# Performance work log

Measured on AMD Instinct MI355X. Metric: run time of the kernel, lower is better.

The kernel has to match this reference:

```python
import jax, jax.numpy as jnp
import numpy as np

N_NODES = 100000
N_EDGES = 3200000


def gcn_conv(x, src, dst, W, b, num_nodes):
    """PyG-style GCNConv: symmetric-normalized aggregation with self-loops."""
    h = x @ W  # [N, out]
    # add self loops
    loop = jnp.arange(num_nodes, dtype=src.dtype)
    s = jnp.concatenate([src, loop])
    d = jnp.concatenate([dst, loop])
    deg = jax.ops.segment_sum(jnp.ones_like(d, dtype=h.dtype), d, num_segments=num_nodes)
    dinv = jnp.where(deg > 0, jax.lax.rsqrt(deg), 0.0)
    norm = dinv[s] * dinv[d]  # [E+N]
    msg = h[s] * norm[:, None]  # gather + scale
    out = jax.ops.segment_sum(msg, d, num_segments=num_nodes)  # scatter-add
    return out + b


def setup_inputs() -> dict:
    key = jax.random.key(0)
    ks = jax.random.split(key, 8)
    x = jax.random.normal(ks[0], (N_NODES, 8), dtype=jnp.float32)
    edge_index = jax.random.randint(ks[1], (2, N_EDGES), 0, N_NODES, dtype=jnp.int64)
    W1 = jax.random.normal(ks[2], (8, 64), dtype=jnp.float32) * 0.3
    b1 = jnp.zeros((64,), dtype=jnp.float32)
    W2 = jax.random.normal(ks[3], (64, 32), dtype=jnp.float32) * 0.12
    b2 = jnp.zeros((32,), dtype=jnp.float32)
    conv_w = jax.random.normal(ks[4], (16, 32, 3), dtype=jnp.float32) * 0.1
    conv_b = jnp.zeros((16,), dtype=jnp.float32)
    fc_w = jax.random.normal(ks[5], (16, 22), dtype=jnp.float32) * 0.25
    fc_b = jnp.zeros((22,), dtype=jnp.float32)
    return {"x": x, "edge_index": edge_index, "W1": W1, "b1": b1, "W2": W2,
            "b2": b2, "conv_w": conv_w, "conv_b": conv_b, "fc_w": fc_w, "fc_b": fc_b}


def reference(x, edge_index, W1, b1, W2, b2, conv_w, conv_b, fc_w, fc_b):
    src, dst = edge_index[0], edge_index[1]
    h = jax.nn.elu(gcn_conv(x, src, dst, W1, b1, N_NODES))   # [N, 64]
    h = jax.nn.elu(gcn_conv(h, src, dst, W2, b2, N_NODES))   # [N, 32]
    # Conv1d(32,16,3) over the node axis: [1, C=32, L=N]
    hc = h.T[None]  # [1, 32, N]
    y = jax.lax.conv_general_dilated(hc, conv_w, window_strides=(1,),
                                     padding='VALID',
                                     dimension_numbers=('NCH', 'OIH', 'NCH'))
    y = jax.nn.relu(y + conv_b[None, :, None])  # [1, 16, N-2]
    y = y[0].T  # [N-2, 16]
    return y @ fc_w + fc_b  # [N-2, 22]
```

## Files before the change

kernel.cpp:

```cpp
#include <hip/hip_runtime.h>
#include <hip/hip_fp16.h>
#include <math.h>

#define BKT_SHIFT 8
#define BKT_NODES 256
#define HROWS 64

__global__ __launch_bounds__(256) void k_hist(const int* __restrict__ dst,
                                              int* __restrict__ bcnt, int E, int NB) {
    __shared__ int lh[512];
    for (int i = threadIdx.x; i < NB; i += 256) lh[i] = 0;
    __syncthreads();
    int base = blockIdx.x * 4096;
    if (base + 4096 <= E) {
        const int4* d4 = (const int4*)(dst + base);
#pragma unroll
        for (int k = 0; k < 4; ++k) {
            int4 v = d4[k * 256 + threadIdx.x];
            atomicAdd(&lh[v.x >> BKT_SHIFT], 1);
            atomicAdd(&lh[v.y >> BKT_SHIFT], 1);
            atomicAdd(&lh[v.z >> BKT_SHIFT], 1);
            atomicAdd(&lh[v.w >> BKT_SHIFT], 1);
        }
    } else {
        for (int k = 0; k < 16; ++k) {
            int i = base + k * 256 + threadIdx.x;
            if (i < E) atomicAdd(&lh[dst[i] >> BKT_SHIFT], 1);
        }
    }
    __syncthreads();
    for (int i = threadIdx.x; i < NB; i += 256)
        if (lh[i]) atomicAdd(&bcnt[i], lh[i]);
}

__global__ __launch_bounds__(512) void k_bscan(const int* __restrict__ bc,
                                               int* __restrict__ boff,
                                               int* __restrict__ bcur, int NB, int E) {
    __shared__ int s[512];
    __shared__ int carry;
    if (threadIdx.x == 0) carry = 0;
    __syncthreads();
    for (int base = 0; base < NB; base += 512) {
        int i = base + threadIdx.x;
        int v = (i < NB) ? bc[i] : 0;
        s[threadIdx.x] = v;
        __syncthreads();
        for (int off = 1; off < 512; off <<= 1) {
            int t = (threadIdx.x >= off) ? s[threadIdx.x - off] : 0;
            __syncthreads();
            s[threadIdx.x] += t;
            __syncthreads();
        }
        if (i < NB) {
            int ex = carry + s[threadIdx.x] - v;
            boff[i] = ex;
            bcur[i] = ex;
        }
        __syncthreads();
        if (threadIdx.x == 0) carry += s[511];
        __syncthreads();
    }
    if (threadIdx.x == 0) boff[NB] = E;
}

__global__ __launch_bounds__(1024) void k_part(const int* __restrict__ src,
                                               const int* __restrict__ dst,
                                               int* __restrict__ bcur,
                                               int* __restrict__ ebuf, int E, int NB) {
    __shared__ int lh[512];
    for (int i = threadIdx.x; i < NB; i += 1024) lh[i] = 0;
    __syncthreads();
    int base = blockIdx.x * 8192;
    if (base + 8192 <= E) {
        const int4* d4 = (const int4*)(dst + base);
#pragma unroll
        for (int k = 0; k < 2; ++k) {
            int4 v = d4[k * 1024 + threadIdx.x];
            atomicAdd(&lh[v.x >> BKT_SHIFT], 1);
            atomicAdd(&lh[v.y >> BKT_SHIFT], 1);
            atomicAdd(&lh[v.z >> BKT_SHIFT], 1);
            atomicAdd(&lh[v.w >> BKT_SHIFT], 1);
        }
    } else {
        for (int k = 0; k < 8; ++k) {
            int i = base + k * 1024 + threadIdx.x;
            if (i < E) atomicAdd(&lh[dst[i] >> BKT_SHIFT], 1);
        }
    }
    __syncthreads();
    for (int t = threadIdx.x; t < NB; t += 1024) {
        int c = lh[t];
        lh[t] = c ? atomicAdd(&bcur[t], c) : 0;
    }
    __syncthreads();
    if (base + 8192 <= E) {
        const int4* d4 = (const int4*)(dst + base);
        const int4* s4 = (const int4*)(src + base);
#pragma unroll
        for (int k = 0; k < 2; ++k) {
            int4 dv = d4[k * 1024 + threadIdx.x];
            int4 sv = s4[k * 1024 + threadIdx.x];
            int p;
            p = atomicAdd(&lh[dv.x >> BKT_SHIFT], 1); ebuf[p] = ((dv.x & 255) << 24) | sv.x;
            p = atomicAdd(&lh[dv.y >> BKT_SHIFT], 1); ebuf[p] = ((dv.y & 255) << 24) | sv.y;
            p = atomicAdd(&lh[dv.z >> BKT_SHIFT], 1); ebuf[p] = ((dv.z & 255) << 24) | sv.z;
            p = atomicAdd(&lh[dv.w >> BKT_SHIFT], 1); ebuf[p] = ((dv.w & 255) << 24) | sv.w;
        }
    } else {
        for (int k = 0; k < 8; ++k) {
            int i = base + k * 1024 + threadIdx.x;
            if (i < E) {
                int d = dst[i];
                int p = atomicAdd(&lh[d >> BKT_SHIFT], 1);
                ebuf[p] = ((d & 255) << 24) | src[i];
            }
        }
    }
}

__global__ __launch_bounds__(256) void k_lsort(const int* __restrict__ boff,
                                               const int* __restrict__ ebuf,
                                               const float* __restrict__ x,
                                               int* __restrict__ rowstart,
                                               float* __restrict__ dinv,
                                               __half2* __restrict__ hx,
                                               int* __restrict__ csr, int n, int NB) {
    __shared__ int off[256];
    __shared__ int cnt[256];
    int b = blockIdx.x;
    int start = boff[b], end = boff[b + 1];
    cnt[threadIdx.x] = 0;
    __syncthreads();
    for (int i = start + threadIdx.x; i < end; i += 256)
        atomicAdd(&cnt[((unsigned)ebuf[i]) >> 24], 1);
    __syncthreads();
    int v = cnt[threadIdx.x];
    off[threadIdx.x] = v;
    __syncthreads();
    for (int o = 1; o < 256; o <<= 1) {
        int t = (threadIdx.x >= o) ? off[threadIdx.x - o] : 0;
        __syncthreads();
        off[threadIdx.x] += t;
        __syncthreads();
    }
    int excl = off[threadIdx.x] - v;
    int node = (b << BKT_SHIFT) + threadIdx.x;
    if (node < n) {
        rowstart[node] = start + excl;
        float dv = rsqrtf((float)v + 1.0f);
        dinv[node] = dv;
        const float4* xp = (const float4*)(x + (size_t)node * 8);
        float4 a = xp[0], c = xp[1];
        __half2* hp = hx + (size_t)node * 4;
        hp[0] = __floats2half2_rn(a.x * dv, a.y * dv);
        hp[1] = __floats2half2_rn(a.z * dv, a.w * dv);
        hp[2] = __floats2half2_rn(c.x * dv, c.y * dv);
        hp[3] = __floats2half2_rn(c.z * dv, c.w * dv);
    }
    __syncthreads();
    off[threadIdx.x] = excl;
    __syncthreads();
    for (int i = start + threadIdx.x; i < end; i += 256) {
        int rec = ebuf[i];
        int d = ((unsigned)rec) >> 24;
        int pos = atomicAdd(&off[d], 1);
        csr[start + pos] = rec & 0xFFFFFF;
    }
    if (b == NB - 1 && threadIdx.x == 0) rowstart[n] = end;
}

__global__ __launch_bounds__(256) void k_agg1g(const int* __restrict__ rs, const int* __restrict__ csr,
                                               const float* __restrict__ dinv, const __half2* __restrict__ hx,
                                               const float* __restrict__ W1, const float* __restrict__ bias,
                                               const float* __restrict__ W2, __half* __restrict__ hw2, int n) {
    __shared__ float w[512];
    __shared__ float sb[64];
    __shared__ float w2s[64 * 36];
    for (int i = threadIdx.x; i < 512; i += 256) w[i] = W1[i];
    if (threadIdx.x < 64) sb[threadIdx.x] = bias[threadIdx.x];
    for (int i = threadIdx.x; i < 2048; i += 256) {
        int r = i >> 5, c = i & 31;
        w2s[r * 36 + c] = W2[i];
    }
    __syncthreads();
    int wid = (blockIdx.x * 256 + threadIdx.x) >> 2;
    if (wid >= n) return;
    int jp = threadIdx.x & 3;
    int start = rs[wid], end = rs[wid + 1];
    float ax = 0.f, ay = 0.f;
    for (int i = start; i < end; i += 16) {
        int idx[16];
        float msk[16];
#pragma unroll
        for (int k = 0; k < 16; ++k) {
            int ii = i + k;
            bool ok = ii < end;
            idx[k] = ok ? csr[ii] : wid;
            msk[k] = ok ? 1.f : 0.f;
        }
        float2 f[16];
#pragma unroll
        for (int k = 0; k < 16; ++k)
            f[k] = __half22float2(hx[((size_t)idx[k] << 2) + jp]);
#pragma unroll
        for (int k = 0; k < 16; ++k) {
            ax = fmaf(msk[k], f[k].x, ax);
            ay = fmaf(msk[k], f[k].y, ay);
        }
    }
    {
        float2 f = __half22float2(hx[((size_t)wid << 2) + jp]);
        ax += f.x; ay += f.y;
    }
    float bx = __shfl_xor(ax, 1), by = __shfl_xor(ay, 1);
    float cx = __shfl_xor(ax, 2), cy = __shfl_xor(ay, 2);
    float dx = __shfl_xor(bx, 2), dy = __shfl_xor(by, 2);
    float dv = dinv[wid];
    int fb = jp * 16;
    const float* r0 = &w[(2 * jp) * 64 + fb];          const float* r1 = r0 + 64;
    const float* r2 = &w[(2 * (jp ^ 1)) * 64 + fb];    const float* r3 = r2 + 64;
    const float* r4 = &w[(2 * (jp ^ 2)) * 64 + fb];    const float* r5 = r4 + 64;
    const float* r6 = &w[(2 * (jp ^ 3)) * 64 + fb];    const float* r7 = r6 + 64;
    const float* sbp = &sb[fb];
    float4 o4[4];
#pragma unroll
    for (int m4 = 0; m4 < 4; ++m4) {
        float4 wa = *(const float4*)&r0[m4 * 4];
        float4 wb = *(const float4*)&r1[m4 * 4];
        float4 wc = *(const float4*)&r2[m4 * 4];
        float4 wd = *(const float4*)&r3[m4 * 4];
        float4 we = *(const float4*)&r4[m4 * 4];
        float4 wf = *(const float4*)&r5[m4 * 4];
        float4 wg = *(const float4*)&r6[m4 * 4];
        float4 wh = *(const float4*)&r7[m4 * 4];
        float4 o;
        o.x = dv * (ax * wa.x + ay * wb.x + bx * wc.x + by * wd.x + cx * we.x + cy * wf.x + dx * wg.x + dy * wh.x) + sbp[m4 * 4 + 0];
        o.y = dv * (ax * wa.y + ay * wb.y + bx * wc.y + by * wd.y + cx * we.y + cy * wf.y + dx * wg.y + dy * wh.y) + sbp[m4 * 4 + 1];
        o.z = dv * (ax * wa.z + ay * wb.z + bx * wc.z + by * wd.z + cx * we.z + cy * wf.z + dx * wg.z + dy * wh.z) + sbp[m4 * 4 + 2];
        o.w = dv * (ax * wa.w + ay * wb.w + bx * wc.w + by * wd.w + cx * we.w + cy * wf.w + dx * wg.w + dy * wh.w) + sbp[m4 * 4 + 3];
        o.x = o.x > 0.f ? o.x : expm1f(o.x);
        o.y = o.y > 0.f ? o.y : expm1f(o.y);
        o.z = o.z > 0.f ? o.z : expm1f(o.z);
        o.w = o.w > 0.f ? o.w : expm1f(o.w);
        o4[m4] = o;
    }
    float4 acc[8];
#pragma unroll
    for (int j4 = 0; j4 < 8; ++j4) acc[j4] = make_float4(0.f, 0.f, 0.f, 0.f);
#pragma unroll
    for (int m4 = 0; m4 < 4; ++m4) {
        int mm = (m4 + jp) & 3;
        float4 ov;
        {
            float4 t0 = (mm & 2) ? o4[2] : o4[0];
            float4 t1 = (mm & 2) ? o4[3] : o4[1];
            ov = (mm & 1) ? t1 : t0;
        }
#pragma unroll
        for (int q = 0; q < 4; ++q) {
            float om = q == 0 ? ov.x : q == 1 ? ov.y : q == 2 ? ov.z : ov.w;
            const float4* wr = (const float4*)&w2s[(fb + mm * 4 + q) * 36];
#pragma unroll
            for (int j4 = 0; j4 < 8; ++j4) {
                float4 wv = wr[j4];
                acc[j4].x = fmaf(om, wv.x, acc[j4].x);
                acc[j4].y = fmaf(om, wv.y, acc[j4].y);
                acc[j4].z = fmaf(om, wv.z, acc[j4].z);
                acc[j4].w = fmaf(om, wv.w, acc[j4].w);
            }
        }
    }
    bool hi1 = (jp & 1) != 0;
    float4 keep1[4];
#pragma unroll
    for (int i = 0; i < 4; ++i) {
        float4 lo = acc[i], hi = acc[i + 4];
        float4 mine, send;
        mine.x = hi1 ? hi.x : lo.x;  send.x = hi1 ? lo.x : hi.x;
        mine.y = hi1 ? hi.y : lo.y;  send.y = hi1 ? lo.y : hi.y;
        mine.z = hi1 ? hi.z : lo.z;  send.z = hi1 ? lo.z : hi.z;
        mine.w = hi1 ? hi.w : lo.w;  send.w = hi1 ? lo.w : hi.w;
        mine.x += __shfl_xor(send.x, 1);
        mine.y += __shfl_xor(send.y, 1);
        mine.z += __shfl_xor(send.z, 1);
        mine.w += __shfl_xor(send.w, 1);
        keep1[i] = mine;
    }
    bool hi2 = (jp & 2) != 0;
    float4 fin[2];
#pragma unroll
    for (int i = 0; i < 2; ++i) {
        float4 lo = keep1[i], hi = keep1[i + 2];
        float4 mine, send;
        mine.x = hi2 ? hi.x : lo.x;  send.x = hi2 ? lo.x : hi.x;
        mine.y = hi2 ? hi.y : lo.y;  send.y = hi2 ? lo.y : hi.y;
        mine.z = hi2 ? hi.z : lo.z;  send.z = hi2 ? lo.z : hi.z;
        mine.w = hi2 ? hi.w : lo.w;  send.w = hi2 ? lo.w : hi.w;
        mine.x += __shfl_xor(send.x, 2);
        mine.y += __shfl_xor(send.y, 2);
        mine.z += __shfl_xor(send.z, 2);
        mine.w += __shfl_xor(send.w, 2);
        fin[i] = mine;
    }
    int jb = (jp & 1) * 16 + (jp & 2) * 4;
    __half2 h01 = __floats2half2_rn(fin[0].x * dv, fin[0].y * dv);
    __half2 h23 = __floats2half2_rn(fin[0].z * dv, fin[0].w * dv);
    __half2 h45 = __floats2half2_rn(fin[1].x * dv, fin[1].y * dv);
    __half2 h67 = __floats2half2_rn(fin[1].z * dv, fin[1].w * dv);
    uint4 u;
    u.x = *(unsigned*)&h01; u.y = *(unsigned*)&h23;
    u.z = *(unsigned*)&h45; u.w = *(unsigned*)&h67;
    *(uint4*)((char*)hw2 + (size_t)wid * 64 + jb * 2) = u;
}

__global__ __launch_bounds__(256) void k_aggr32p(const int* __restrict__ rs, const int* __restrict__ csr,
                                                 const float* __restrict__ dinv, const __half* __restrict__ hw,
                                                 const float* __restrict__ bias, float* __restrict__ g, int n) {
    int wid = (blockIdx.x * 256 + threadIdx.x) >> 4;
    if (wid >= n) return;
    int j = threadIdx.x & 15;
    int start = rs[wid], end = rs[wid + 1];
    const __half2* hp = (const __half2*)hw;
    float ax = 0.f, ay = 0.f;
    for (int i = start; i < end; i += 16) {
        int idx[16];
        float msk[16];
#pragma unroll
        for (int k = 0; k < 16; ++k) {
            int ii = i + k;
            bool ok = ii < end;
            idx[k] = ok ? csr[ii] : wid;
            msk[k] = ok ? 1.f : 0.f;
        }
        float2 f[16];
#pragma unroll
        for (int k = 0; k < 16; ++k)
            f[k] = __half22float2(hp[((size_t)idx[k] << 4) + j]);
#pragma unroll
        for (int k = 0; k < 16; ++k) {
            ax = fmaf(msk[k], f[k].x, ax);
            ay = fmaf(msk[k], f[k].y, ay);
        }
    }
    float dv = dinv[wid];
    float2 fs = __half22float2(hp[((size_t)wid << 4) + j]);
    float2 bb = ((const float2*)bias)[j];
    float vx = dv * (ax + fs.x) + bb.x;
    float vy = dv * (ay + fs.y) + bb.y;
    float2 r;
    r.x = vx > 0.f ? vx : expm1f(vx);
    r.y = vy > 0.f ? vy : expm1f(vy);
    ((float2*)(g + ((size_t)wid << 5)))[j] = r;
}

__global__ __launch_bounds__(256) void k_head(const float* __restrict__ g2, const float* __restrict__ cw,
                                              const float* __restrict__ cb, const float* __restrict__ fw,
                                              const float* __restrict__ fb, float* __restrict__ out,
                                              int nrows) {
    __shared__ float tile[(HROWS + 2) * 36];
    __shared__ float scwT[96 * 16];
    __shared__ float ytile[HROWS * 20];
    __shared__ float sfwT[22 * 16];
    __shared__ float scb[16], sfb[22];
    int base = blockIdx.x * HROWS;
    int rcnt = nrows - base; if (rcnt > HROWS) rcnt = HROWS;
    for (int i = threadIdx.x; i < 1536; i += 256) {
        int co = i / 96, rem = i - co * 96;
        scwT[rem * 16 + co] = cw[i];
    }
    for (int i = threadIdx.x; i < 352; i += 256) {
        int co = i / 22, col = i - co * 22;
        sfwT[col * 16 + co] = fw[i];
    }
    if (threadIdx.x < 16) scb[threadIdx.x] = cb[threadIdx.x];
    if (threadIdx.x < 22) sfb[threadIdx.x] = fb[threadIdx.x];
    int nload4 = (rcnt + 2) * 8;
    for (int i = threadIdx.x; i < nload4; i += 256) {
        int r = i >> 3, c4 = i & 7;
        float4 v = *(const float4*)(g2 + (size_t)(base + r) * 32 + c4 * 4);
        *(float4*)&tile[r * 36 + c4 * 4] = v;
    }
    __syncthreads();
    int r = threadIdx.x >> 2;
    int c0 = threadIdx.x & 3;
    if (r < rcnt) {
        float4 acc = { scb[c0 * 4], scb[c0 * 4 + 1], scb[c0 * 4 + 2], scb[c0 * 4 + 3] };
#pragma unroll
        for (int k = 0; k < 3; ++k) {
            const float* tr = &tile[(r + k) * 36];
#pragma unroll
            for (int ci4 = 0; ci4 < 8; ++ci4) {
                float4 xv = *(const float4*)&tr[ci4 * 4];
#pragma unroll
                for (int q = 0; q < 4; ++q) {
                    int ci = ci4 * 4 + q;
                    float4 wv = *(const float4*)&scwT[(ci * 3 + k) * 16 + c0 * 4];
                    float xq = q == 0 ? xv.x : q == 1 ? xv.y : q == 2 ? xv.z : xv.w;
                    acc.x += xq * wv.x;
                    acc.y += xq * wv.y;
                    acc.z += xq * wv.z;
                    acc.w += xq * wv.w;
                }
            }
        }
        float4 yv;
        yv.x = acc.x > 0.f ? acc.x : 0.f;
        yv.y = acc.y > 0.f ? acc.y : 0.f;
        yv.z = acc.z > 0.f ? acc.z : 0.f;
        yv.w = acc.w > 0.f ? acc.w : 0.f;
        *(float4*)&ytile[r * 20 + c0 * 4] = yv;
    }
    __syncthreads();
    int items = rcnt * 22;
    for (int it = threadIdx.x; it < items; it += 256) {
        int row = it / 22, col = it - row * 22;
        const float* yr = &ytile[row * 20];
        const float* wc = &sfwT[col * 16];
        float s = sfb[col];
#pragma unroll
        for (int co4 = 0; co4 < 4; ++co4) {
            float4 yv = *(const float4*)&yr[co4 * 4];
            float4 wv = *(const float4*)&wc[co4 * 4];
            s += yv.x * wv.x + yv.y * wv.y + yv.z * wv.z + yv.w * wv.w;
        }
        out[(size_t)base * 22 + it] = s;
    }
}

extern "C" void kernel_launch(void* const* d_in, const int* in_sizes, int n_in,
                              void* d_out, int out_size, void* d_ws, size_t ws_size,
                              hipStream_t stream) {
    const float* x  = (const float*)d_in[0];
    const int*   ei = (const int*)d_in[1];
    const float* W1 = (const float*)d_in[2];
    const float* b1 = (const float*)d_in[3];
    const float* W2 = (const float*)d_in[4];
    const float* b2 = (const float*)d_in[5];
    const float* cw = (const float*)d_in[6];
    const float* cb = (const float*)d_in[7];
    const float* fw = (const float*)d_in[8];
    const float* fb = (const float*)d_in[9];
    float* out = (float*)d_out;

    int N = in_sizes[0] / 8;
    int E = in_sizes[1] / 2;
    const int* src = ei;
    const int* dst = ei + E;
    int NB = (N + BKT_NODES - 1) >> BKT_SHIFT;

    auto alignB = [](size_t v) { return (v + 1023) & ~(size_t)1023; };
    char* wsb = (char*)d_ws;
    size_t o = 0;
    int* bcnt = (int*)(wsb + o);      o += 2048;
    int* boff = (int*)(wsb + o);      o += 2048;
    int* bcur = (int*)(wsb + o);      o += 2048;
    int* rowstart = (int*)(wsb + o);  o += alignB((size_t)(N + 1) * 4);
    float* dinv = (float*)(wsb + o);  o += alignB((size_t)N * 4);
    int* csr = (int*)(wsb + o);       o += alignB((size_t)E * 4 + 256);
    __half2* hx = (__half2*)(wsb + o);  o += alignB((size_t)N * 8 * 2);
    __half* hw2 = (__half*)(wsb + o);   o += alignB((size_t)N * 32 * 2);
    float* B = (float*)(wsb + o);     o += (size_t)N * 64 * 4;
    int* ebuf = (int*)B;

    hipMemsetAsync(bcnt, 0, (size_t)NB * sizeof(int), stream);
    k_hist<<<(E + 4095) / 4096, 256, 0, stream>>>(dst, bcnt, E, NB);
    k_bscan<<<1, 512, 0, stream>>>(bcnt, boff, bcur, NB, E);
    k_part<<<(E + 8191) / 8192, 1024, 0, stream>>>(src, dst, bcur, ebuf, E, NB);
    k_lsort<<<NB, 256, 0, stream>>>(boff, ebuf, x, rowstart, dinv, hx, csr, N, NB);

    k_agg1g<<<(int)(((size_t)N * 4 + 255) / 256), 256, 0, stream>>>(rowstart, csr, dinv, hx, W1, b1, W2, hw2, N);

    k_aggr32p<<<(int)(((size_t)N * 16 + 255) / 256), 256, 0, stream>>>(rowstart, csr, dinv, hw2, b2, B, N);

    k_head<<<(N - 2 + HROWS - 1) / HROWS, 256, 0, stream>>>(B, cw, cb, fw, fb, out, N - 2);
}
```

Baseline: 172.1 us.

## Fuse second GCN aggregation with conv1d and FC head kernel

```diff
diff --git a/kernel.cpp b/kernel.cpp
--- a/kernel.cpp
+++ b/kernel.cpp
@@ -4,7 +4,7 @@
 
 #define BKT_SHIFT 8
 #define BKT_NODES 256
-#define HROWS 64
+#define HB 16
 
 __global__ __launch_bounds__(256) void k_hist(const int* __restrict__ dst,
                                               int* __restrict__ bcnt, int E, int NB) {
@@ -313,106 +313,85 @@
     *(uint4*)((char*)hw2 + (size_t)wid * 64 + jb * 2) = u;
 }
 
-__global__ __launch_bounds__(256) void k_aggr32p(const int* __restrict__ rs, const int* __restrict__ csr,
-                                                 const float* __restrict__ dinv, const __half* __restrict__ hw,
-                                                 const float* __restrict__ bias, float* __restrict__ g, int n) {
-    int wid = (blockIdx.x * 256 + threadIdx.x) >> 4;
-    if (wid >= n) return;
-    int j = threadIdx.x & 15;
-    int start = rs[wid], end = rs[wid + 1];
-    const __half2* hp = (const __half2*)hw;
-    float ax = 0.f, ay = 0.f;
-    for (int i = start; i < end; i += 16) {
-        int idx[16];
-        float msk[16];
-#pragma unroll
-        for (int k = 0; k < 16; ++k) {
-            int ii = i + k;
-            bool ok = ii < end;
-            idx[k] = ok ? csr[ii] : wid;
-            msk[k] = ok ? 1.f : 0.f;
-        }
-        float2 f[16];
-#pragma unroll
-        for (int k = 0; k < 16; ++k)
-            f[k] = __half22float2(hp[((size_t)idx[k] << 4) + j]);
-#pragma unroll
-        for (int k = 0; k < 16; ++k) {
-            ax = fmaf(msk[k], f[k].x, ax);
-            ay = fmaf(msk[k], f[k].y, ay);
-        }
-    }
-    float dv = dinv[wid];
-    float2 fs = __half22float2(hp[((size_t)wid << 4) + j]);
-    float2 bb = ((const float2*)bias)[j];
-    float vx = dv * (ax + fs.x) + bb.x;
-    float vy = dv * (ay + fs.y) + bb.y;
-    float2 r;
-    r.x = vx > 0.f ? vx : expm1f(vx);
-    r.y = vy > 0.f ? vy : expm1f(vy);
-    ((float2*)(g + ((size_t)wid << 5)))[j] = r;
-}
-
-__global__ __launch_bounds__(256) void k_head(const float* __restrict__ g2, const float* __restrict__ cw,
-                                              const float* __restrict__ cb, const float* __restrict__ fw,
-                                              const float* __restrict__ fb, float* __restrict__ out,
-                                              int nrows) {
-    __shared__ float tile[(HROWS + 2) * 36];
+__global__ __launch_bounds__(320) void k_agg2h(const int* __restrict__ rs, const int* __restrict__ csr,
+                                               const float* __restrict__ dinv, const __half* __restrict__ hw,
+                                               const float* __restrict__ bias,
+                                               const float* __restrict__ cw, const float* __restrict__ cb,
+                                               const float* __restrict__ fw, const float* __restrict__ fb,
+                                               float* __restrict__ out, int n, int nrows) {
+    __shared__ float tile[18 * 36];
     __shared__ float scwT[96 * 16];
-    __shared__ float ytile[HROWS * 20];
+    __shared__ float ytile[16 * 20];
     __shared__ float sfwT[22 * 16];
-    __shared__ float scb[16], sfb[22];
-    int base = blockIdx.x * HROWS;
-    int rcnt = nrows - base; if (rcnt > HROWS) rcnt = HROWS;
-    for (int i = threadIdx.x; i < 1536; i += 256) {
+    __shared__ float scb[16], sfb[22], sbb[32];
+    for (int i = threadIdx.x; i < 1536; i += 320) {
         int co = i / 96, rem = i - co * 96;
         scwT[rem * 16 + co] = cw[i];
     }
-    for (int i = threadIdx.x; i < 352; i += 256) {
+    for (int i = threadIdx.x; i < 352; i += 320) {
         int co = i / 22, col = i - co * 22;
         sfwT[col * 16 + co] = fw[i];
     }
     if (threadIdx.x < 16) scb[threadIdx.x] = cb[threadIdx.x];
     if (threadIdx.x < 22) sfb[threadIdx.x] = fb[threadIdx.x];
-    int nload4 = (rcnt + 2) * 8;
-    for (int i = threadIdx.x; i < nload4; i += 256) {
-        int r = i >> 3, c4 = i & 7;
-        float4 v = *(const float4*)(g2 + (size_t)(base + r) * 32 + c4 * 4);
-        *(float4*)&tile[r * 36 + c4 * 4] = v;
-    }
-    __syncthreads();
-    int r = threadIdx.x >> 2;
-    int c0 = threadIdx.x & 3;
-    if (r < rcnt) {
-        float4 acc = { scb[c0 * 4], scb[c0 * 4 + 1], scb[c0 * 4 + 2], scb[c0 * 4 + 3] };
-#pragma unroll
-        for (int k = 0; k < 3; ++k) {
-            const float* tr = &tile[(r + k) * 36];
-#pragma unroll
-            for (int ci4 = 0; ci4 < 8; ++ci4) {
-                float4 xv = *(const float4*)&tr[ci4 * 4];
-#pragma unroll
-                for (int q = 0; q < 4; ++q) {
-                    int ci = ci4 * 4 + q;
-                    float4 wv = *(const float4*)&scwT[(ci * 3 + k) * 16 + c0 * 4];
-                    float xq = q == 0 ? xv.x : q == 1 ? xv.y : q == 2 ? xv.z : xv.w;
-                    acc.x += xq * wv.x;
-                    acc.y += xq * wv.y;
-                    acc.z += xq * wv.z;
-                    acc.w += xq * wv.w;
-                }
+    if (threadIdx.x < 32) sbb[threadIdx.x] = bias[threadIdx.x];
+    __syncthreads();
+    int base = blockIdx.x * HB;
+    int slot = threadIdx.x >> 4;
+    int j = threadIdx.x & 15;
+    int wid = base + slot;
+    if (slot < 18 && wid < n) {
+        int start = rs[wid], end = rs[wid + 1];
+        const __half2* hp = (const __half2*)hw;
+        float ax = 0.f, ay = 0.f;
+        for (int i = start; i < end; i += 16) {
+            int idx[16];
+            float msk[16];
+#pragma unroll
+            for (int k = 0; k < 16; ++k) {
+                int ii = i + k;
+                bool ok = ii < end;
+                idx[k] = ok ? csr[ii] : wid;
+                msk[k] = ok ? 1.f : 0.f;
             }
-        }
-        float4 yv;
-        yv.x = acc.x > 0.f ? acc.x : 0.f;
-        yv.y = acc.y > 0.f ? acc.y : 0.f;
-        yv.z = acc.z > 0.f ? acc.z : 0.f;
-        yv.w = acc.w > 0.f ? acc.w : 0.f;
-        *(float4*)&ytile[r * 20 + c0 * 4] = yv;
+            float2 f[16];
+#pragma unroll
+            for (int k = 0; k < 16; ++k)
+                f[k] = __half22float2(hp[((size_t)idx[k] << 4) + j]);
+#pragma unroll
+            for (int k = 0; k < 16; ++k) {
+                ax = fmaf(msk[k], f[k].x, ax);
+                ay = fmaf(msk[k], f[k].y, ay);
+            }
+        }
+        float dv = dinv[wid];
+        float2 fs = __half22float2(hp[((size_t)wid << 4) + j]);
+        float vx = dv * (ax + fs.x) + sbb[2 * j];
+        float vy = dv * (ay + fs.y) + sbb[2 * j + 1];
+        vx = vx > 0.f ? vx : expm1f(vx);
+        vy = vy > 0.f ? vy : expm1f(vy);
+        tile[slot * 36 + 2 * j]     = vx;
+        tile[slot * 36 + 2 * j + 1] = vy;
+    }
+    __syncthreads();
+    int rcnt = nrows - base; if (rcnt > HB) rcnt = HB;
+    if (threadIdx.x < 256) {
+        int r = threadIdx.x >> 4, co = threadIdx.x & 15;
+        if (r < rcnt) {
+            float acc = scb[co];
+#pragma unroll
+            for (int k = 0; k < 3; ++k) {
+                const float* tr = &tile[(r + k) * 36];
+#pragma unroll
+                for (int ci = 0; ci < 32; ++ci)
+                    acc = fmaf(tr[ci], scwT[(ci * 3 + k) * 16 + co], acc);
+            }
+            ytile[r * 20 + co] = acc > 0.f ? acc : 0.f;
+        }
     }
     __syncthreads();
     int items = rcnt * 22;
-    for (int it = threadIdx.x; it < items; it += 256) {
+    for (int it = threadIdx.x; it < items; it += 320) {
         int row = it / 22, col = it - row * 22;
         const float* yr = &ytile[row * 20];
         const float* wc = &sfwT[col * 16];
@@ -459,8 +438,7 @@
     int* csr = (int*)(wsb + o);       o += alignB((size_t)E * 4 + 256);
     __half2* hx = (__half2*)(wsb + o);  o += alignB((size_t)N * 8 * 2);
     __half* hw2 = (__half*)(wsb + o);   o += alignB((size_t)N * 32 * 2);
-    float* B = (float*)(wsb + o);     o += (size_t)N * 64 * 4;
-    int* ebuf = (int*)B;
+    int* ebuf = (int*)(wsb + o);      o += alignB((size_t)E * 4);
 
     hipMemsetAsync(bcnt, 0, (size_t)NB * sizeof(int), stream);
     k_hist<<<(E + 4095) / 4096, 256, 0, stream>>>(dst, bcnt, E, NB);
@@ -470,7 +448,7 @@
 
     k_agg1g<<<(int)(((size_t)N * 4 + 255) / 256), 256, 0, stream>>>(rowstart, csr, dinv, hx, W1, b1, W2, hw2, N);
 
-    k_aggr32p<<<(int)(((size_t)N * 16 + 255) / 256), 256, 0, stream>>>(rowstart, csr, dinv, hw2, b2, B, N);
-
-    k_head<<<(N - 2 + HROWS - 1) / HROWS, 256, 0, stream>>>(B, cw, cb, fw, fb, out, N - 2);
-}
+    int nrows = N - 2;
+    k_agg2h<<<(nrows + HB - 1) / HB, 320, 0, stream>>>(rowstart, csr, dinv, hw2, b2,
+                                                       cw, cb, fw, fb, out, N, nrows);
+}
```

Result: slower. 207.3 us (+20.5%).
